# Optimization experiments

Hardware: AMD Instinct MI355X
Metric: run time of the kernel (lower is better)

Reference implementation:

```python
import jax, jax.numpy as jnp
import numpy as np

L, D, V = 8, 1024, 32000
DT_MIN, DT_MAX = 0.01, 0.1
EPS = 1e-5


def _layer_norm(x, w, b):
    mu = jnp.mean(x, -1, keepdims=True)
    var = jnp.var(x, -1, keepdims=True)
    return (x - mu) * jax.lax.rsqrt(var + EPS) * w + b


def _encode(ids):
    # deterministic phase encoding of tokens onto the unit phase sphere
    theta = 2.0 * jnp.pi * ids.astype(jnp.float32) / V  # [B,S]
    k = jnp.arange(1, D // 2 + 1, dtype=jnp.float32)
    ang = theta[..., None] * k  # [B,S,D/2]
    return jnp.concatenate([jnp.cos(ang), jnp.sin(ang)], -1) / jnp.sqrt(jnp.float32(D))


def _flux(s, mask):
    # attention-like causal score from state self-interaction
    score = jnp.einsum('bqd,bkd->bqk', s, s) / jnp.sqrt(jnp.float32(D))
    score = jnp.where(mask, score, 0.0)
    return jnp.einsum('bqk,bkd->bqd', score, s), score


def _evolve_with_tunneling(s, dt, mask):
    # Heun-Euler (predictor-corrector) integration step
    k1, score = _flux(s, mask)
    mid = s + dt * k1
    k2, _ = _flux(mid, mask)
    ev = s + 0.5 * dt * (k1 + k2)
    # quantum tunneling: boost low-energy states proportionally to dt/dt_max
    energy = jnp.linalg.norm(ev, axis=-1)  # [B,S]
    thr = jnp.mean(energy, axis=-1, keepdims=True)
    tunnel = energy < thr
    strength = dt / DT_MAX  # [B,1,1]
    ev = jnp.where(tunnel[..., None], ev * (1.0 + strength), ev)
    ratio = jnp.mean(tunnel.astype(jnp.float32))
    return ev, score, ratio


def setup_inputs() -> dict:
    key = jax.random.key(0)
    ks = jax.random.split(key, 4)
    B, S = 2, 2048
    input_ids = jax.random.randint(ks[0], (B, S), 0, V)
    labels = jax.random.randint(ks[1], (B, S), 0, V)
    proj_w = jax.random.normal(ks[2], (L, D, D), jnp.float32) * 0.02
    proj_b = jnp.zeros((L, D), jnp.float32)
    ln_w = jnp.ones((L, D), jnp.float32)
    ln_b = jnp.zeros((L, D), jnp.float32)
    fln_w = jnp.ones((D,), jnp.float32)
    fln_b = jnp.zeros((D,), jnp.float32)
    out_w = jax.random.normal(ks[3], (D, V), jnp.float32) * 0.02
    return dict(input_ids=input_ids, labels=labels, proj_w=proj_w, proj_b=proj_b,
                ln_w=ln_w, ln_b=ln_b, fln_w=fln_w, fln_b=fln_b, out_w=out_w)


def reference(input_ids, labels, proj_w, proj_b, ln_w, ln_b, fln_w, fln_b, out_w):
    B, S = input_ids.shape
    mask = jnp.tril(jnp.ones((S, S), dtype=bool))
    # deterministic timestep (midpoint of [dt_min, dt_max]); dropout in eval mode
    dt = jnp.full((B, 1, 1), 0.5 * (DT_MIN + DT_MAX), jnp.float32)
    states = _encode(input_ids)
    for i in range(L):
        ev, _score, _ratio = _evolve_with_tunneling(states, dt, mask)
        states = _layer_norm(ev @ proj_w[i] + proj_b[i], ln_w[i], ln_b[i])
    states = _layer_norm(states, fln_w, fln_b)
    # normalized quantum projection to vocab
    energy = jnp.linalg.norm(states, axis=-1, keepdims=True)
    logits = (states / (energy + 1e-12)) @ out_w  # [B,S,V]
    # shifted cross-entropy
    sl = logits[:, :-1, :].reshape(-1, V)
    tl = labels[:, 1:].reshape(-1)
    logp = jax.nn.log_softmax(sl, axis=-1)
    loss = -jnp.mean(jnp.take_along_axis(logp, tl[:, None], axis=1))
    return logits, loss
```

## Files before the change

### kernel.cpp

```cpp
#include <hip/hip_runtime.h>

#define LL 8
#define DD 1024
#define VV 32000
#define SS 2048
#define BB 2
#define NROWS 4096
#define DT_STEP 0.055f
#define HALF_DT 0.0275f
#define TUNNEL_SCALE 1.55f

typedef __attribute__((ext_vector_type(8))) short bf16x8;
typedef __attribute__((ext_vector_type(4))) float f32x4;

static __device__ __forceinline__ float bf2f(unsigned short u){
  union { unsigned int i; float f; } v; v.i = ((unsigned int)u) << 16; return v.f;
}
static __device__ __forceinline__ unsigned short f2bf(float f){
  union { float f; unsigned int i; } v; v.f = f;
  unsigned int r = v.i + 0x7fffu + ((v.i >> 16) & 1u);
  return (unsigned short)(r >> 16);
}

static __device__ __forceinline__ void gl16(const unsigned short* g, unsigned short* l){
  __builtin_amdgcn_global_load_lds(
      (const __attribute__((address_space(1))) unsigned int*)g,
      (__attribute__((address_space(3))) unsigned int*)l, 16, 0, 0);
}

__device__ __forceinline__ float block_sum256(float v, volatile float* scratch){
  #pragma unroll
  for (int off = 32; off; off >>= 1) v += __shfl_down(v, off, 64);
  int w = threadIdx.x >> 6, lane = threadIdx.x & 63;
  __syncthreads();
  if (lane == 0) scratch[w] = v;
  __syncthreads();
  return scratch[0] + scratch[1] + scratch[2] + scratch[3];
}

__global__ void encode_kernel(const int* __restrict__ ids, float* __restrict__ s_f32,
                              unsigned short* __restrict__ hi, unsigned short* __restrict__ lo){
  int row = blockIdx.x;
  int t = threadIdx.x;
  float theta = 6.28318530717958647692f * (float)ids[row] / 32000.0f;
  #pragma unroll
  for (int i = 0; i < 2; ++i){
    int kk = t + i * 256;
    float ang = theta * (float)(kk + 1);
    float sv, cv; sincosf(ang, &sv, &cv);
    float c = cv * 0.03125f, s = sv * 0.03125f;
    long b0 = (long)row * DD + kk, b1 = b0 + 512;
    s_f32[b0] = c; s_f32[b1] = s;
    unsigned short ch = f2bf(c); hi[b0] = ch; lo[b0] = f2bf(c - bf2f(ch));
    unsigned short sh = f2bf(s); hi[b1] = sh; lo[b1] = f2bf(s - bf2f(sh));
  }
}

__global__ void transpose_bf16_pair_kernel(const unsigned short* __restrict__ in_hi,
                                           const unsigned short* __restrict__ in_lo,
                                           unsigned short* __restrict__ out_hi,
                                           unsigned short* __restrict__ out_lo,
                                           int R, int C){
  __shared__ __align__(16) unsigned short tile[64][80];
  int zz = blockIdx.z;
  const unsigned short* in = (zz & 1) ? in_lo : in_hi;
  unsigned short* out = (zz & 1) ? out_lo : out_hi;
  long ib = (long)(zz >> 1) * R * C;
  int c0 = blockIdx.x * 64, r0 = blockIdx.y * 64;
  int t = threadIdx.x;
  #pragma unroll
  for (int i = 0; i < 2; ++i){
    int j = t + i * 256; int row = j >> 3, cc = j & 7;
    *(uint4*)&tile[row][cc * 8] = *(const uint4*)(in + ib + (long)(r0 + row) * C + c0 + cc * 8);
  }
  __syncthreads();
  #pragma unroll
  for (int i = 0; i < 2; ++i){
    int j = t + i * 256; int orow = j >> 3, cc = j & 7;
    union { unsigned short u[8]; uint4 v; } tmp;
    #pragma unroll
    for (int e = 0; e < 8; ++e) tmp.u[e] = tile[cc * 8 + e][orow];
    *(uint4*)(out + ib + (long)(c0 + orow) * R + r0 + cc * 8) = tmp.v;
  }
}

template<bool SPLIT>
__global__ void transpose_f32_bf16_kernel(const float* __restrict__ in,
                                          unsigned short* __restrict__ ohi,
                                          unsigned short* __restrict__ olo, int R, int C){
  __shared__ float tile[64][68];
  long ib = (long)blockIdx.z * R * C;
  int c0 = blockIdx.x * 64, r0 = blockIdx.y * 64;
  int t = threadIdx.x;
  #pragma unroll
  for (int i = 0; i < 4; ++i){
    int j = t + i * 256; int row = j >> 4, cc = j & 15;
    *(float4*)&tile[row][cc * 4] = *(const float4*)(in + ib + (long)(r0 + row) * C + c0 + cc * 4);
  }
  __syncthreads();
  #pragma unroll
  for (int i = 0; i < 2; ++i){
    int j = t + i * 256; int orow = j >> 3, cc = j & 7;
    union { unsigned short u[8]; uint4 v; } th, tl;
    #pragma unroll
    for (int e = 0; e < 8; ++e){
      float v = tile[cc * 8 + e][orow];
      unsigned short h = f2bf(v); th.u[e] = h;
      if (SPLIT) tl.u[e] = f2bf(v - bf2f(h));
    }
    long ob = ib + (long)(c0 + orow) * R + r0 + cc * 8;
    *(uint4*)(ohi + ob) = th.v;
    if (SPLIT) *(uint4*)(olo + ob) = tl.v;
  }
}

template<int OUTMODE, int CAUSAL>
__global__ __launch_bounds__(512, 4)
void gemm_nt_kernel(const unsigned short* __restrict__ Ahi, const unsigned short* __restrict__ Alo,
                    const unsigned short* __restrict__ Bhi, const unsigned short* __restrict__ Blo,
                    float* __restrict__ C, unsigned short* __restrict__ Chi,
                    unsigned short* __restrict__ Clo, const float* __restrict__ bias,
                    int K, int lda, int ldb, int ldc, int MT, int NT,
                    long batchA, long batchB, long batchC, float alpha)
{
  const int bz = blockIdx.y;
  int mt, nt, ks = 0;
  {
    const int nwg = (CAUSAL == 4) ? (MT * NT * 2) : (MT * NT);
    const int q = nwg >> 3, r = nwg & 7;
    const int xcd = blockIdx.x & 7, off = blockIdx.x >> 3;
    const int wg = (xcd < r ? xcd * (q + 1) : r * (q + 1) + (xcd - r) * q) + off;
    if (CAUSAL == 3){
      if (wg < 128){ ks = 0; mt = wg >> 3; nt = wg & 7; }
      else { int w2 = wg - 128; ks = 1; mt = 8 + (w2 >> 3); nt = w2 & 7; }
    } else if (CAUSAL == 4){
      int w2 = wg; ks = 0;
      if (w2 >= MT * NT){ ks = 1; w2 -= MT * NT; }
      mt = w2 / NT; nt = w2 - mt * NT;
    } else {
      const int band = wg / (NT << 3), rem = wg - band * (NT << 3);
      mt = (band << 3) + (rem & 7); nt = rem >> 3;
    }
  }
  if (CAUSAL == 1 && nt > mt) return;
  const int m0 = mt << 7, n0 = nt << 7;
  int kstart = 0, kend = K;
  if (CAUSAL == 2){ int kl = (mt + 1) << 7; kend = kl < K ? kl : K; }
  if (CAUSAL == 3){
    kstart = ks << 10;
    int kl = (mt + 1) << 7, kc = kstart + 1024;
    kend = kl < kc ? kl : kc;
  }
  if (CAUSAL == 4){
    kstart = ks * (K >> 1);
    kend = kstart + (K >> 1);
  }

  __shared__ __align__(16) unsigned short sA[2][128][64];
  __shared__ __align__(16) unsigned short sB[2][128][64];

  const int tid = threadIdx.x;
  const int lane = tid & 63;
  const int w = tid >> 6;
  const int wr = w >> 2, wc = w & 3;
  const int fr = lane & 15, fc = lane >> 4;
  const int fr7 = fr & 7;

  f32x4 acc[4][2];
  #pragma unroll
  for (int i = 0; i < 4; ++i)
    #pragma unroll
    for (int j = 0; j < 2; ++j) acc[i][j] = (f32x4){0.f, 0.f, 0.f, 0.f};

  const int srow = tid >> 3, slot = tid & 7;
  const int cont = slot ^ (srow & 7);
  const long aoff = (long)bz * batchA, boff = (long)bz * batchB;
  const int gcol = (cont & 3) << 3;
  const unsigned short* gA = (cont >= 4 ? Alo : Ahi) + aoff + (long)(m0 + srow) * lda + gcol;
  const unsigned short* gB = (cont >= 4 ? Blo : Bhi) + boff + (long)(n0 + srow) * ldb + gcol;
  const long rstepA = 64L * lda, rstepB = 64L * ldb;
  const int wofs = w << 9;

  const int oh = (fc ^ fr7) << 4;
  const int ol = ((4 + fc) ^ fr7) << 4;

  const int ntiles = (kend - kstart) >> 5;

  gl16(gA + kstart,          &sA[0][0][0] + wofs);
  gl16(gA + kstart + rstepA, &sA[0][0][0] + 4096 + wofs);
  gl16(gB + kstart,          &sB[0][0][0] + wofs);
  gl16(gB + kstart + rstepB, &sB[0][0][0] + 4096 + wofs);

  int cur = 0;
  for (int t = 0; t < ntiles; ++t){
    const bool stg = (t < ntiles - 1);
    const long nk = kstart + ((long)(t + 1) << 5);
    const char* bA_ = (const char*)&sA[cur][0][0];
    const char* bB_ = (const char*)&sB[cur][0][0];
    bf16x8 ah_[4], al_[4];

    if (stg){
      gl16(gA + nk,          &sA[cur ^ 1][0][0] + wofs);
      gl16(gA + nk + rstepA, &sA[cur ^ 1][0][0] + 4096 + wofs);
      asm volatile("s_waitcnt vmcnt(2)" ::: "memory");
    } else {
      asm volatile("s_waitcnt vmcnt(0)" ::: "memory");
    }
    asm volatile("s_barrier" ::: "memory");
    #pragma unroll
    for (int mi = 0; mi < 4; ++mi){
      const char* p_ = bA_ + (wr * 64 + mi * 16 + fr) * 128;
      ah_[mi] = *(const bf16x8*)(p_ + oh);
      al_[mi] = *(const bf16x8*)(p_ + ol);
    }
    {
      const char* pb_ = bB_ + (wc * 32 + fr) * 128;
      bf16x8 bh_ = *(const bf16x8*)(pb_ + oh);
      bf16x8 bl_ = *(const bf16x8*)(pb_ + ol);
      __builtin_amdgcn_s_setprio(1);
      #pragma unroll
      for (int mi = 0; mi < 4; ++mi){
        acc[mi][0] = __builtin_amdgcn_mfma_f32_16x16x32_bf16(ah_[mi], bh_, acc[mi][0], 0, 0, 0);
        acc[mi][0] = __builtin_amdgcn_mfma_f32_16x16x32_bf16(ah_[mi], bl_, acc[mi][0], 0, 0, 0);
        acc[mi][0] = __builtin_amdgcn_mfma_f32_16x16x32_bf16(al_[mi], bh_, acc[mi][0], 0, 0, 0);
      }
      __builtin_amdgcn_s_setprio(0);
    }

    if (stg){
      gl16(gB + nk,          &sB[cur ^ 1][0][0] + wofs);
      gl16(gB + nk + rstepB, &sB[cur ^ 1][0][0] + 4096 + wofs);
    }
    asm volatile("s_barrier" ::: "memory");
    {
      const char* pb_ = bB_ + (wc * 32 + 16 + fr) * 128;
      bf16x8 bh_ = *(const bf16x8*)(pb_ + oh);
      bf16x8 bl_ = *(const bf16x8*)(pb_ + ol);
      __builtin_amdgcn_s_setprio(1);
      #pragma unroll
      for (int mi = 0; mi < 4; ++mi){
        acc[mi][1] = __builtin_amdgcn_mfma_f32_16x16x32_bf16(ah_[mi], bh_, acc[mi][1], 0, 0, 0);
        acc[mi][1] = __builtin_amdgcn_mfma_f32_16x16x32_bf16(ah_[mi], bl_, acc[mi][1], 0, 0, 0);
        acc[mi][1] = __builtin_amdgcn_mfma_f32_16x16x32_bf16(al_[mi], bh_, acc[mi][1], 0, 0, 0);
      }
      __builtin_amdgcn_s_setprio(0);
    }
    cur ^= 1;
  }

  const long coff = (long)bz * batchC;
  float* Cout = ((OUTMODE == 5 || CAUSAL == 4) && ks) ? (float*)Chi : C;
  const int rb0 = m0 + wr * 64 + fc * 4;
  const int cb0 = n0 + wc * 32 + fr;
  #pragma unroll
  for (int mi = 0; mi < 4; ++mi){
    #pragma unroll
    for (int ni = 0; ni < 2; ++ni){
      #pragma unroll
      for (int rg = 0; rg < 4; ++rg){
        int row = rb0 + mi * 16 + rg;
        int col = cb0 + ni * 16;
        float v = acc[mi][ni][rg] * alpha;
        long idx = coff + (long)row * ldc + col;
        if (OUTMODE == 0){
          if (bias && ks == 0) v += bias[col];
          Cout[idx] = v;
        } else if (OUTMODE == 2){
          if (CAUSAL == 1 && col > row) v = 0.0f;
          unsigned short h = f2bf(v);
          Chi[idx] = h;
          Clo[idx] = f2bf(v - bf2f(h));
        } else {
          Cout[idx] = v;
        }
      }
    }
  }
}

__global__ __launch_bounds__(512, 4)
void gemm256_kernel(const unsigned short* __restrict__ A,
                    const unsigned short* __restrict__ Bt,
                    float* __restrict__ C,
                    float* __restrict__ psum)
{
  const int MT = 32, NT = 250;
  const int nwg = MT * NT;
  const int q = nwg >> 3;
  const int xcd = blockIdx.x & 7, off = blockIdx.x >> 3;
  const int wg = xcd * q + off;
  const int band = wg / (NT << 3), rem = wg - band * (NT << 3);
  const int mt = (band << 3) + (rem & 7), nt = rem >> 3;
  const int m0 = mt << 7, n0 = nt << 7;

  __shared__ __align__(16) unsigned short sA[2][128][64];
  __shared__ __align__(16) unsigned short sB[2][128][64];

  const int tid = threadIdx.x;
  const int lane = tid & 63;
  const int w = tid >> 6;
  const int wr = w >> 1, wc = w & 1;
  const int fr = lane & 15, fc = lane >> 4;
  const int fr7 = fr & 7;

  f32x4 acc[2][4];
  #pragma unroll
  for (int i = 0; i < 2; ++i)
    #pragma unroll
    for (int j = 0; j < 4; ++j) acc[i][j] = (f32x4){0.f, 0.f, 0.f, 0.f};

  const int srow = tid >> 3, slot = tid & 7;
  const int cont = slot ^ (srow & 7);
  const unsigned short* gA = A  + (long)(m0 + srow) * DD + (cont << 3);
  const unsigned short* gB = Bt + (long)(n0 + srow) * DD + (cont << 3);
  const long rstep = 64L * DD;
  const int wofs = w << 9;

  const int oh = (fc ^ fr7) << 4;
  const int ol = ((4 + fc) ^ fr7) << 4;

  gl16(gA,         &sA[0][0][0] + wofs);
  gl16(gA + rstep, &sA[0][0][0] + 4096 + wofs);
  gl16(gB,         &sB[0][0][0] + wofs);
  gl16(gB + rstep, &sB[0][0][0] + 4096 + wofs);

  int cur = 0;
  for (int t = 0; t < 16; ++t){
    const bool stg = (t < 15);
    const long nk = (long)(t + 1) << 6;
    const char* bA_ = (const char*)&sA[cur][0][0];
    const char* bB_ = (const char*)&sB[cur][0][0];
    bf16x8 aq[2][2], bq[4][2];

    if (stg){
      gl16(gA + nk,         &sA[cur ^ 1][0][0] + wofs);
      gl16(gA + nk + rstep, &sA[cur ^ 1][0][0] + 4096 + wofs);
      asm volatile("s_waitcnt vmcnt(2)" ::: "memory");
    } else {
      asm volatile("s_waitcnt vmcnt(0)" ::: "memory");
    }
    asm volatile("s_barrier" ::: "memory");
    #pragma unroll
    for (int mi = 0; mi < 2; ++mi){
      const char* p = bA_ + (wr * 32 + mi * 16 + fr) * 128;
      aq[mi][0] = *(const bf16x8*)(p + oh);
      aq[mi][1] = *(const bf16x8*)(p + ol);
    }
    #pragma unroll
    for (int ni = 0; ni < 2; ++ni){
      const char* p = bB_ + (wc * 64 + ni * 16 + fr) * 128;
      bq[ni][0] = *(const bf16x8*)(p + oh);
      bq[ni][1] = *(const bf16x8*)(p + ol);
    }
    __builtin_amdgcn_s_setprio(1);
    #pragma unroll
    for (int ks = 0; ks < 2; ++ks)
      #pragma unroll
      for (int mi = 0; mi < 2; ++mi)
        #pragma unroll
        for (int ni = 0; ni < 2; ++ni)
          acc[mi][ni] = __builtin_amdgcn_mfma_f32_16x16x32_bf16(aq[mi][ks], bq[ni][ks], acc[mi][ni], 0, 0, 0);
    __builtin_amdgcn_s_setprio(0);

    if (stg){
      gl16(gB + nk,         &sB[cur ^ 1][0][0] + wofs);
      gl16(gB + nk + rstep, &sB[cur ^ 1][0][0] + 4096 + wofs);
    }
    asm volatile("s_barrier" ::: "memory");
    #pragma unroll
    for (int ni = 2; ni < 4; ++ni){
      const char* p = bB_ + (wc * 64 + ni * 16 + fr) * 128;
      bq[ni][0] = *(const bf16x8*)(p + oh);
      bq[ni][1] = *(const bf16x8*)(p + ol);
    }
    __builtin_amdgcn_s_setprio(1);
    #pragma unroll
    for (int ks = 0; ks < 2; ++ks)
      #pragma unroll
      for (int mi = 0; mi < 2; ++mi)
        #pragma unroll
        for (int ni = 2; ni < 4; ++ni)
          acc[mi][ni] = __builtin_amdgcn_mfma_f32_16x16x32_bf16(aq[mi][ks], bq[ni][ks], acc[mi][ni], 0, 0, 0);
    __builtin_amdgcn_s_setprio(0);

    cur ^= 1;
  }

  const int rb0 = m0 + wr * 32 + fc * 4;
  const int cb0 = n0 + wc * 64 + fr;
  #pragma unroll
  for (int mi = 0; mi < 2; ++mi){
    #pragma unroll
    for (int ni = 0; ni < 4; ++ni){
      #pragma unroll
      for (int rg = 0; rg < 4; ++rg){
        C[(long)(rb0 + mi * 16 + rg) * VV + cb0 + ni * 16] = acc[mi][ni][rg];
      }
    }
  }

  #pragma unroll
  for (int mi = 0; mi < 2; ++mi){
    #pragma unroll
    for (int rg = 0; rg < 4; ++rg){
      float s4 = __expf(acc[mi][0][rg]) + __expf(acc[mi][1][rg])
               + __expf(acc[mi][2][rg]) + __expf(acc[mi][3][rg]);
      #pragma unroll
      for (int o = 1; o < 16; o <<= 1) s4 += __shfl_xor(s4, o, 64);
      if (fr == 0){
        long pidx = ((long)(rb0 + mi * 16 + rg) << 9) + nt * 2 + wc;
        psum[pidx] = s4;
      }
    }
  }
}

__global__ void mid_trans_kernel(const float* __restrict__ s, float* __restrict__ k1,
                                 const float* __restrict__ k1b,
                                 unsigned short* __restrict__ ohi, unsigned short* __restrict__ olo,
                                 unsigned short* __restrict__ thi, unsigned short* __restrict__ tlo){
  __shared__ float tile[64][68];
  int c0 = blockIdx.x * 64, r0g = blockIdx.y * 64;
  int t = threadIdx.x;
  #pragma unroll
  for (int i = 0; i < 4; ++i){
    int j = t + i * 256; int row = j >> 4, cc = (j & 15) * 4;
    long idx = (long)(r0g + row) * DD + c0 + cc;
    float4 a = *(const float4*)(k1 + idx);
    if (((r0g + row) & 2047) >= 1024){
      float4 b = *(const float4*)(k1b + idx);
      a.x += b.x; a.y += b.y; a.z += b.z; a.w += b.w;
    }
    *(float4*)(k1 + idx) = a;
    float4 sv = *(const float4*)(s + idx);
    float4 m;
    m.x = sv.x + DT_STEP * a.x; m.y = sv.y + DT_STEP * a.y;
    m.z = sv.z + DT_STEP * a.z; m.w = sv.w + DT_STEP * a.w;
    *(float4*)&tile[row][cc] = m;
    ushort4 hv, lv;
    hv.x = f2bf(m.x); lv.x = f2bf(m.x - bf2f(hv.x));
    hv.y = f2bf(m.y); lv.y = f2bf(m.y - bf2f(hv.y));
    hv.z = f2bf(m.z); lv.z = f2bf(m.z - bf2f(hv.z));
    hv.w = f2bf(m.w); lv.w = f2bf(m.w - bf2f(hv.w));
    *(ushort4*)(ohi + idx) = hv; *(ushort4*)(olo + idx) = lv;
  }
  __syncthreads();
  long tb = (long)(r0g >> 11) * DD * SS;
  int sb = r0g & 2047;
  #pragma unroll
  for (int i = 0; i < 2; ++i){
    int j = t + i * 256; int ocol = j >> 3, cc = (j & 7) * 8;
    union { unsigned short u[8]; uint4 v; } th, tl;
    #pragma unroll
    for (int e = 0; e < 8; ++e){
      float v = tile[cc + e][ocol];
      unsigned short h = f2bf(v);
      th.u[e] = h; tl.u[e] = f2bf(v - bf2f(h));
    }
    long ob = tb + (long)(c0 + ocol) * SS + sb + cc;
    *(uint4*)(thi + ob) = th.v;
    *(uint4*)(tlo + ob) = tl.v;
  }
}

__global__ void ev_energy_kernel(const float* __restrict__ s, const float* __restrict__ k1,
                                 float* __restrict__ k2, const float* __restrict__ k2b,
                                 float* __restrict__ energy){
  int row = blockIdx.x, t = threadIdx.x;
  long base = (long)row * DD + t * 4;
  float4 sv = *(const float4*)(s + base);
  float4 av = *(const float4*)(k1 + base);
  float4 bv = *(const float4*)(k2 + base);
  if ((row & 2047) >= 1024){
    float4 cv = *(const float4*)(k2b + base);
    bv.x += cv.x; bv.y += cv.y; bv.z += cv.z; bv.w += cv.w;
  }
  float4 ev;
  ev.x = sv.x + HALF_DT * (av.x + bv.x);
  ev.y = sv.y + HALF_DT * (av.y + bv.y);
  ev.z = sv.z + HALF_DT * (av.z + bv.z);
  ev.w = sv.w + HALF_DT * (av.w + bv.w);
  *(float4*)(k2 + base) = ev;
  __shared__ float scratch[4];
  float n2 = block_sum256(ev.x*ev.x + ev.y*ev.y + ev.z*ev.z + ev.w*ev.w, scratch);
  if (t == 0) energy[row] = sqrtf(n2);
}

__global__ void tunnel_kernel(const float* __restrict__ ev, const float* __restrict__ energy,
                              unsigned short* __restrict__ hi, unsigned short* __restrict__ lo){
  int row = blockIdx.x, t = threadIdx.x;
  const float* eb = energy + (row >> 11) * SS;
  float s = 0.f;
  for (int j = t; j < SS; j += 256) s += eb[j];
  __shared__ float scratch[4];
  float thr = block_sum256(s, scratch) * (1.0f / SS);
  float scale = (energy[row] < thr) ? TUNNEL_SCALE : 1.0f;
  long base = (long)row * DD + t * 4;
  float4 v = *(const float4*)(ev + base);
  v.x *= scale; v.y *= scale; v.z *= scale; v.w *= scale;
  ushort4 hv, lv;
  hv.x = f2bf(v.x); lv.x = f2bf(v.x - bf2f(hv.x));
  hv.y = f2bf(v.y); lv.y = f2bf(v.y - bf2f(hv.y));
  hv.z = f2bf(v.z); lv.z = f2bf(v.z - bf2f(hv.z));
  hv.w = f2bf(v.w); lv.w = f2bf(v.w - bf2f(hv.w));
  *(ushort4*)(hi + base) = hv; *(ushort4*)(lo + base) = lv;
}

__global__ void ln_kernel(const float* __restrict__ h, const float* __restrict__ hb,
                          const float* __restrict__ w,
                          const float* __restrict__ b, float* __restrict__ s_f32,
                          unsigned short* __restrict__ hi, unsigned short* __restrict__ lo){
  int row = blockIdx.x, t = threadIdx.x;
  long base = (long)row * DD + t * 4;
  float4 xv = *(const float4*)(h + base);
  float4 xb = *(const float4*)(hb + base);
  xv.x += xb.x; xv.y += xb.y; xv.z += xb.z; xv.w += xb.w;
  __shared__ float scratch[4];
  float sum = block_sum256(xv.x + xv.y + xv.z + xv.w, scratch);
  float ssq = block_sum256(xv.x*xv.x + xv.y*xv.y + xv.z*xv.z + xv.w*xv.w, scratch);
  float mu = sum * (1.0f / DD);
  float var = ssq * (1.0f / DD) - mu * mu;
  float rstd = rsqrtf(var + 1e-5f);
  float4 wv = *(const float4*)(w + t * 4), bv = *(const float4*)(b + t * 4);
  float y0 = (xv.x - mu) * rstd * wv.x + bv.x;
  float y1 = (xv.y - mu) * rstd * wv.y + bv.y;
  float y2 = (xv.z - mu) * rstd * wv.z + bv.z;
  float y3 = (xv.w - mu) * rstd * wv.w + bv.w;
  float4 o; o.x = y0; o.y = y1; o.z = y2; o.w = y3;
  *(float4*)(s_f32 + base) = o;
  ushort4 hv, lv;
  hv.x = f2bf(y0); lv.x = f2bf(y0 - bf2f(hv.x));
  hv.y = f2bf(y1); lv.y = f2bf(y1 - bf2f(hv.y));
  hv.z = f2bf(y2); lv.z = f2bf(y2 - bf2f(hv.z));
  hv.w = f2bf(y3); lv.w = f2bf(y3 - bf2f(hv.w));
  *(ushort4*)(hi + base) = hv; *(ushort4*)(lo + base) = lv;
}

__global__ void fln_kernel(const float* __restrict__ s, const float* __restrict__ w,
                           const float* __restrict__ b, unsigned short* __restrict__ uhi){
  int row = blockIdx.x, t = threadIdx.x;
  long base = (long)row * DD + t * 4;
  float4 xv = *(const float4*)(s + base);
  __shared__ float scratch[4];
  float sum = block_sum256(xv.x + xv.y + xv.z + xv.w, scratch);
  float ssq = block_sum256(xv.x*xv.x + xv.y*xv.y + xv.z*xv.z + xv.w*xv.w, scratch);
  float mu = sum * (1.0f / DD);
  float var = ssq * (1.0f / DD) - mu * mu;
  float rstd = rsqrtf(var + 1e-5f);
  float4 wv = *(const float4*)(w + t * 4), bv = *(const float4*)(b + t * 4);
  float y0 = (xv.x - mu) * rstd * wv.x + bv.x;
  float y1 = (xv.y - mu) * rstd * wv.y + bv.y;
  float y2 = (xv.z - mu) * rstd * wv.z + bv.z;
  float y3 = (xv.w - mu) * rstd * wv.w + bv.w;
  float n2 = block_sum256(y0*y0 + y1*y1 + y2*y2 + y3*y3, scratch);
  float inv = 1.0f / (sqrtf(n2) + 1e-12f);
  ushort4 o;
  o.x = f2bf(y0 * inv); o.y = f2bf(y1 * inv);
  o.z = f2bf(y2 * inv); o.w = f2bf(y3 * inv);
  *(ushort4*)(uhi + base) = o;
}

__global__ void lse_reduce_kernel(const float* __restrict__ psum,
                                  const float* __restrict__ logits, const int* __restrict__ labels,
                                  float* __restrict__ lrow){
  int idx = blockIdx.x;
  int b = idx / (SS - 1), qq = idx - b * (SS - 1);
  int row = b * SS + qq;
  int t = threadIdx.x;
  float l = 0.f;
  for (int p = t; p < 500; p += 64) l += psum[((long)row << 9) + p];
  #pragma unroll
  for (int o = 1; o < 64; o <<= 1) l += __shfl_xor(l, o, 64);
  if (t == 0){
    float lse = __logf(l);
    float tl = logits[(long)row * VV + labels[row + 1]];
    lrow[idx] = lse - tl;
  }
}

__global__ void loss_reduce_kernel(const float* __restrict__ lrow, float* __restrict__ dst){
  __shared__ float scratch[4];
  float s = 0.f;
  for (int j = threadIdx.x; j < BB * (SS - 1); j += 256) s += lrow[j];
  float tot = block_sum256(s, scratch);
  if (threadIdx.x == 0) dst[0] = tot / (float)(BB * (SS - 1));
}

extern "C" void kernel_launch(void* const* d_in, const int* in_sizes, int n_in,
                              void* d_out, int out_size, void* d_ws, size_t ws_size,
                              hipStream_t stream) {
  const int*   ids    = (const int*)d_in[0];
  const int*   labels = (const int*)d_in[1];
  const float* proj_w = (const float*)d_in[2];
  const float* proj_b = (const float*)d_in[3];
  const float* ln_w   = (const float*)d_in[4];
  const float* ln_b   = (const float*)d_in[5];
  const float* fln_w  = (const float*)d_in[6];
  const float* fln_b  = (const float*)d_in[7];
  const float* out_w  = (const float*)d_in[8];
  float* out = (float*)d_out;

  char* ws = (char*)d_ws;
  float*          s_f32 = (float*)(ws + 0);
  unsigned short* op_hi = (unsigned short*)(ws + 16777216);
  unsigned short* op_lo = (unsigned short*)(ws + 25165824);
  unsigned short* T_hi  = (unsigned short*)(ws + 33554432);
  unsigned short* T_lo  = (unsigned short*)(ws + 41943040);
  float*          k1    = (float*)(ws + 50331648);
  float*          k2    = (float*)(ws + 67108864);
  unsigned short* sc_hi = (unsigned short*)(ws + 83886080);
  unsigned short* sc_lo = (unsigned short*)(ws + 92274688);
  unsigned short* WhiT  = (unsigned short*)(ws + 100663296);
  unsigned short* WloT  = (unsigned short*)(ws + 117440512);
  float*          energy= (float*)(ws + 134217728);
  float*          lrow  = (float*)(ws + 134234368);
  unsigned short* owT   = T_hi;
  float*          psum  = (float*)(ws + 0);
  float*          k1b   = k2;
  float*          k2b   = (float*)(ws + 16777216);
  float*          hb    = k2;

  transpose_f32_bf16_kernel<true><<<dim3(16, 16, 8), 256, 0, stream>>>(proj_w, WhiT, WloT, DD, DD);
  encode_kernel<<<NROWS, 256, 0, stream>>>(ids, s_f32, op_hi, op_lo);
  transpose_bf16_pair_kernel<<<dim3(16, 32, 4), 256, 0, stream>>>(op_hi, op_lo, T_hi, T_lo, SS, DD);

  for (int l = 0; l < LL; ++l){
    gemm_nt_kernel<2, 1><<<dim3(256, 2), 512, 0, stream>>>(
        op_hi, op_lo, op_hi, op_lo, nullptr, sc_hi, sc_lo, nullptr,
        DD, DD, DD, SS, 16, 16, (long)SS * DD, (long)SS * DD, (long)SS * SS, 0.03125f);
    gemm_nt_kernel<5, 3><<<dim3(192, 2), 512, 0, stream>>>(
        sc_hi, sc_lo, T_hi, T_lo, k1, (unsigned short*)k1b, nullptr, nullptr,
        SS, SS, SS, DD, 24, 8, (long)SS * SS, (long)DD * SS, (long)SS * DD, 1.0f);
    mid_trans_kernel<<<dim3(16, 64), 256, 0, stream>>>(s_f32, k1, k1b, op_hi, op_lo, T_hi, T_lo);
    gemm_nt_kernel<2, 1><<<dim3(256, 2), 512, 0, stream>>>(
        op_hi, op_lo, op_hi, op_lo, nullptr, sc_hi, sc_lo, nullptr,
        DD, DD, DD, SS, 16, 16, (long)SS * DD, (long)SS * DD, (long)SS * SS, 0.03125f);
    gemm_nt_kernel<5, 3><<<dim3(192, 2), 512, 0, stream>>>(
        sc_hi, sc_lo, T_hi, T_lo, k2, (unsigned short*)k2b, nullptr, nullptr,
        SS, SS, SS, DD, 24, 8, (long)SS * SS, (long)DD * SS, (long)SS * DD, 1.0f);
    ev_energy_kernel<<<NROWS, 256, 0, stream>>>(s_f32, k1, k2, k2b, energy);
    tunnel_kernel<<<NROWS, 256, 0, stream>>>(k2, energy, op_hi, op_lo);
    gemm_nt_kernel<0, 4><<<dim3(512, 1), 512, 0, stream>>>(
        op_hi, op_lo, WhiT + (long)l * DD * DD, WloT + (long)l * DD * DD,
        k1, (unsigned short*)hb, nullptr, proj_b + l * DD,
        DD, DD, DD, DD, 32, 8, 0, 0, 0, 1.0f);
    ln_kernel<<<NROWS, 256, 0, stream>>>(k1, hb, ln_w + l * DD, ln_b + l * DD, s_f32, op_hi, op_lo);
    if (l < LL - 1){
      transpose_bf16_pair_kernel<<<dim3(16, 32, 4), 256, 0, stream>>>(op_hi, op_lo, T_hi, T_lo, SS, DD);
    }
  }

  transpose_f32_bf16_kernel<false><<<dim3(500, 16, 1), 256, 0, stream>>>(out_w, owT, nullptr, DD, VV);
  fln_kernel<<<NROWS, 256, 0, stream>>>(s_f32, fln_w, fln_b, op_hi);
  gemm256_kernel<<<8000, 512, 0, stream>>>(op_hi, owT, out, psum);
  lse_reduce_kernel<<<BB * (SS - 1), 64, 0, stream>>>(psum, out, labels, lrow);
  loss_reduce_kernel<<<1, 256, 0, stream>>>(lrow, out + (long)NROWS * VV);
}
```

Measured before the change: 2.541 ms.

## Add dedicated causal score kernel computing only lower-triangular 128x64 tiles

Replaces the generic split-bf16 GEMM used for the causal score matrix with a specialised kernel. It launches exactly the 272 128x64 tiles on or below the diagonal per batch, finding each tile's indices with a sqrt-based formula. It double-buffers the A and B tiles in LDS and does hi/lo compensated bf16 MFMA with the causal mask and alpha fused into the epilogue. The aim is to skip work above the diagonal and use a tile shape better suited to K=1024. It relies on the downstream consumer never reading the upper-triangle score tiles, which are no longer written.

Result: faster. 2.401 ms (-5.5%).

```diff
diff --git a/kernel.cpp b/kernel.cpp
--- a/kernel.cpp
+++ b/kernel.cpp
@@ -273,6 +273,129 @@
         } else {
           Cout[idx] = v;
         }
+      }
+    }
+  }
+}
+
+__global__ __launch_bounds__(512, 4)
+void score64_kernel(const unsigned short* __restrict__ Ahi, const unsigned short* __restrict__ Alo,
+                    unsigned short* __restrict__ Chi, unsigned short* __restrict__ Clo,
+                    float alpha)
+{
+  const int bz = blockIdx.y;
+  const int wg = (blockIdx.x & 7) * 34 + (blockIdx.x >> 3);
+  int mt = (int)((sqrtf(4.0f * wg + 1.0f) - 1.0f) * 0.5f);
+  while (mt * mt + mt > wg) --mt;
+  while ((mt + 1) * (mt + 1) + (mt + 1) <= wg) ++mt;
+  const int nt = wg - mt * mt - mt;
+  const int m0 = mt << 7, n0 = nt << 6;
+
+  __shared__ __align__(16) unsigned short sA[2][128][64];
+  __shared__ __align__(16) unsigned short sB[2][64][64];
+
+  const int tid = threadIdx.x;
+  const int lane = tid & 63;
+  const int w = tid >> 6;
+  const int wr = w >> 1, wc = w & 1;
+  const int fr = lane & 15, fc = lane >> 4;
+  const int fr7 = fr & 7;
+
+  f32x4 acc[2][2];
+  #pragma unroll
+  for (int i = 0; i < 2; ++i)
+    #pragma unroll
+    for (int j = 0; j < 2; ++j) acc[i][j] = (f32x4){0.f, 0.f, 0.f, 0.f};
+
+  const int srow = tid >> 3, slot = tid & 7;
+  const int cont = slot ^ (srow & 7);
+  const long boffs = (long)bz * SS * DD;
+  const int gcol = (cont & 3) << 3;
+  const unsigned short* gA = (cont >= 4 ? Alo : Ahi) + boffs + (long)(m0 + srow) * DD + gcol;
+  const unsigned short* gB = (cont >= 4 ? Alo : Ahi) + boffs + (long)(n0 + srow) * DD + gcol;
+  const long rstepA = 64L * DD;
+  const int wofs = w << 9;
+
+  const int oh = (fc ^ fr7) << 4;
+  const int ol = ((4 + fc) ^ fr7) << 4;
+
+  gl16(gA,          &sA[0][0][0] + wofs);
+  gl16(gA + rstepA, &sA[0][0][0] + 4096 + wofs);
+  gl16(gB,          &sB[0][0][0] + wofs);
+
+  int cur = 0;
+  for (int t = 0; t < 32; ++t){
+    const bool stg = (t < 31);
+    const long nk = (long)(t + 1) << 5;
+    const char* bA_ = (const char*)&sA[cur][0][0];
+    const char* bB_ = (const char*)&sB[cur][0][0];
+    bf16x8 ah_[2], al_[2];
+
+    if (stg){
+      gl16(gA + nk,          &sA[cur ^ 1][0][0] + wofs);
+      gl16(gA + nk + rstepA, &sA[cur ^ 1][0][0] + 4096 + wofs);
+      asm volatile("s_waitcnt vmcnt(2)" ::: "memory");
+    } else {
+      asm volatile("s_waitcnt vmcnt(0)" ::: "memory");
+    }
+    asm volatile("s_barrier" ::: "memory");
+    #pragma unroll
+    for (int mi = 0; mi < 2; ++mi){
+      const char* p_ = bA_ + (wr * 32 + mi * 16 + fr) * 128;
+      ah_[mi] = *(const bf16x8*)(p_ + oh);
+      al_[mi] = *(const bf16x8*)(p_ + ol);
+    }
+    {
+      const char* pb_ = bB_ + (wc * 32 + fr) * 128;
+      bf16x8 bh_ = *(const bf16x8*)(pb_ + oh);
+      bf16x8 bl_ = *(const bf16x8*)(pb_ + ol);
+      __builtin_amdgcn_s_setprio(1);
+      #pragma unroll
+      for (int mi = 0; mi < 2; ++mi){
+        acc[mi][0] = __builtin_amdgcn_mfma_f32_16x16x32_bf16(ah_[mi], bh_, acc[mi][0], 0, 0, 0);
+        acc[mi][0] = __builtin_amdgcn_mfma_f32_16x16x32_bf16(ah_[mi], bl_, acc[mi][0], 0, 0, 0);
+        acc[mi][0] = __builtin_amdgcn_mfma_f32_16x16x32_bf16(al_[mi], bh_, acc[mi][0], 0, 0, 0);
+      }
+      __builtin_amdgcn_s_setprio(0);
+    }
+
+    if (stg){
+      gl16(gB + nk, &sB[cur ^ 1][0][0] + wofs);
+    }
+    asm volatile("s_barrier" ::: "memory");
+    {
+      const char* pb_ = bB_ + (wc * 32 + 16 + fr) * 128;
+      bf16x8 bh_ = *(const bf16x8*)(pb_ + oh);
+      bf16x8 bl_ = *(const bf16x8*)(pb_ + ol);
+      __builtin_amdgcn_s_setprio(1);
+      #pragma unroll
+      for (int mi = 0; mi < 2; ++mi){
+        acc[mi][1] = __builtin_amdgcn_mfma_f32_16x16x32_bf16(ah_[mi], bh_, acc[mi][1], 0, 0, 0);
+        acc[mi][1] = __builtin_amdgcn_mfma_f32_16x16x32_bf16(ah_[mi], bl_, acc[mi][1], 0, 0, 0);
+        acc[mi][1] = __builtin_amdgcn_mfma_f32_16x16x32_bf16(al_[mi], bh_, acc[mi][1], 0, 0, 0);
+      }
+      __builtin_amdgcn_s_setprio(0);
+    }
+    cur ^= 1;
+  }
+
+  const long coff = (long)bz * SS * SS;
+  const int rb0 = m0 + wr * 32 + fc * 4;
+  const int cb0 = n0 + wc * 32 + fr;
+  #pragma unroll
+  for (int mi = 0; mi < 2; ++mi){
+    #pragma unroll
+    for (int ni = 0; ni < 2; ++ni){
+      #pragma unroll
+      for (int rg = 0; rg < 4; ++rg){
+        int row = rb0 + mi * 16 + rg;
+        int col = cb0 + ni * 16;
+        float v = acc[mi][ni][rg] * alpha;
+        if (col > row) v = 0.0f;
+        long idx = coff + (long)row * SS + col;
+        unsigned short h = f2bf(v);
+        Chi[idx] = h;
+        Clo[idx] = f2bf(v - bf2f(h));
       }
     }
   }
@@ -625,16 +748,12 @@
   transpose_bf16_pair_kernel<<<dim3(16, 32, 4), 256, 0, stream>>>(op_hi, op_lo, T_hi, T_lo, SS, DD);
 
   for (int l = 0; l < LL; ++l){
-    gemm_nt_kernel<2, 1><<<dim3(256, 2), 512, 0, stream>>>(
-        op_hi, op_lo, op_hi, op_lo, nullptr, sc_hi, sc_lo, nullptr,
-        DD, DD, DD, SS, 16, 16, (long)SS * DD, (long)SS * DD, (long)SS * SS, 0.03125f);
+    score64_kernel<<<dim3(272, 2), 512, 0, stream>>>(op_hi, op_lo, sc_hi, sc_lo, 0.03125f);
     gemm_nt_kernel<5, 3><<<dim3(192, 2), 512, 0, stream>>>(
         sc_hi, sc_lo, T_hi, T_lo, k1, (unsigned short*)k1b, nullptr, nullptr,
         SS, SS, SS, DD, 24, 8, (long)SS * SS, (long)DD * SS, (long)SS * DD, 1.0f);
     mid_trans_kernel<<<dim3(16, 64), 256, 0, stream>>>(s_f32, k1, k1b, op_hi, op_lo, T_hi, T_lo);
-    gemm_nt_kernel<2, 1><<<dim3(256, 2), 512, 0, stream>>>(
-        op_hi, op_lo, op_hi, op_lo, nullptr, sc_hi, sc_lo, nullptr,
-        DD, DD, DD, SS, 16, 16, (long)SS * DD, (long)SS * DD, (long)SS * SS, 0.03125f);
+    score64_kernel<<<dim3(272, 2), 512, 0, stream>>>(op_hi, op_lo, sc_hi, sc_lo, 0.03125f);
     gemm_nt_kernel<5, 3><<<dim3(192, 2), 512, 0, stream>>>(
         sc_hi, sc_lo, T_hi, T_lo, k2, (unsigned short*)k2b, nullptr, nullptr,
         SS, SS, SS, DD, 24, 8, (long)SS * SS, (long)DD * SS, (long)SS * DD, 1.0f);
```
